# Kernel optimization log

Hardware: AMD Instinct MI355X
Metric: run time of the kernel (lower is better)

## Reference

```python
import jax, jax.numpy as jnp
import numpy as np

T, IN, INTER, OUT = 4096, 1024, 1024, 1024

def setup_inputs() -> dict:
    key = jax.random.key(0)
    ks = jax.random.split(key, 11)
    s_in = 1.0 / np.sqrt(IN)
    s_int = 1.0 / np.sqrt(INTER)
    return {
        "x": jax.random.normal(ks[0], (T, IN), dtype=jnp.float32),
        "d_gamma": jax.random.uniform(ks[1], (T, T), dtype=jnp.float32),
        "Wq": jax.random.uniform(ks[2], (IN, INTER), jnp.float32, -s_in, s_in),
        "bq": jax.random.uniform(ks[3], (INTER,), jnp.float32, -s_in, s_in),
        "Wk": jax.random.uniform(ks[4], (IN, INTER), jnp.float32, -s_in, s_in),
        "bk": jax.random.uniform(ks[5], (INTER,), jnp.float32, -s_in, s_in),
        "Wv": jax.random.uniform(ks[6], (IN, INTER), jnp.float32, -s_in, s_in),
        "bv": jax.random.uniform(ks[7], (INTER,), jnp.float32, -s_in, s_in),
        "Wr": jax.random.uniform(ks[8], (INTER, OUT), jnp.float32, -s_int, s_int),
        "br": jax.random.uniform(ks[9], (OUT,), jnp.float32, -s_int, s_int),
        "prelu_a": jnp.asarray(0.25, dtype=jnp.float32),
    }

def reference(x, d_gamma, Wq, bq, Wk, bk, Wv, bv, Wr, br, prelu_a):
    num_node = x.shape[0]
    xr = x.reshape(T, IN)
    q = xr @ Wq + bq                      # [T, INTER]
    k = xr @ Wk + bk                      # [T, INTER]
    v = xr @ Wv + bv                      # [T, INTER]
    scores = q @ k.T                      # [T, T] retention scores
    retained = (d_gamma * scores) @ v     # decay-masked aggregation, [T, INTER]
    out = retained @ Wr + br              # [T, OUT]
    out = jnp.where(out >= 0, out, prelu_a * out)  # PReLU
    return out.reshape(num_node, -1)
```

## Files before the change

### kernel.cpp

```cpp
#include <hip/hip_runtime.h>

#define TT 4096
#define DIN 1024

typedef _Float16 f16;
typedef __attribute__((ext_vector_type(8))) _Float16 f16x8;
typedef __attribute__((ext_vector_type(4))) _Float16 f16x4;
typedef __attribute__((ext_vector_type(4))) float f32x4;

__device__ f16 g_xh[TT * DIN];
__device__ f16 g_wqkvT[3 * DIN * DIN];
__device__ f16 g_wrT[DIN * DIN];
__device__ f16 g_q[TT * DIN];
__device__ f16 g_k[TT * DIN];
__device__ f16 g_v[TT * DIN];
__device__ f16 g_vT[DIN * TT];
__device__ f16 g_sg[(size_t)TT * TT];
__device__ f16 g_part[4][TT * DIN];
__device__ f16 g_ret[TT * DIN];

__global__ __launch_bounds__(256) void prep_cast_x(const float* __restrict__ x) {
    int i = (blockIdx.x * 256 + threadIdx.x) * 8;
    f32x4 a = *(const f32x4*)&x[i];
    f32x4 b = *(const f32x4*)&x[i + 4];
    f16x8 o;
#pragma unroll
    for (int j = 0; j < 4; ++j) { o[j] = (f16)a[j]; o[j + 4] = (f16)b[j]; }
    *(f16x8*)&g_xh[i] = o;
}

__global__ void prep_transpose(const float* __restrict__ Wq, const float* __restrict__ Wk,
                               const float* __restrict__ Wv, const float* __restrict__ Wr) {
    int idx = blockIdx.x * 256 + threadIdx.x;
    int which = blockIdx.y;
    const float* src = (which == 0) ? Wq : (which == 1) ? Wk : (which == 2) ? Wv : Wr;
    f16* dst = (which < 3) ? (g_wqkvT + (size_t)which * DIN * DIN) : g_wrT;
    int j = idx >> 10, k = idx & 1023;
    dst[idx] = (f16)src[k * DIN + j];
}

__global__ __launch_bounds__(256) void transpose_v() {
    __shared__ f16 t[64][72];
    const int bc = blockIdx.x;
    const int br = blockIdx.y;
    const int tdx = threadIdx.x;
    const int r0 = tdx >> 3;
    const int c8 = (tdx & 7) * 8;
#pragma unroll
    for (int p = 0; p < 2; ++p) {
        int r = r0 + p * 32;
        *(f16x8*)&t[r][c8] = *(const f16x8*)&g_v[(size_t)(br * 64 + r) * DIN + bc * 64 + c8];
    }
    __syncthreads();
#pragma unroll
    for (int p = 0; p < 2; ++p) {
        int c = r0 + p * 32;
        f16x8 v;
#pragma unroll
        for (int j = 0; j < 8; ++j) v[j] = t[c8 + j][c];
        *(f16x8*)&g_vT[(size_t)(bc * 64 + c) * TT + br * 64 + c8] = v;
    }
}

__global__ __launch_bounds__(256) void gamma_mult(const float* __restrict__ gamma) {
    const size_t total = (size_t)TT * TT;
    const size_t stride = (size_t)gridDim.x * 256 * 8;
    for (size_t i = ((size_t)blockIdx.x * 256 + threadIdx.x) * 8; i < total; i += stride) {
        f16x8 sv = *(const f16x8*)&g_sg[i];
        f32x4 g0 = *(const f32x4*)&gamma[i];
        f32x4 g1 = *(const f32x4*)&gamma[i + 4];
        f16x8 o;
#pragma unroll
        for (int j = 0; j < 4; ++j) {
            o[j]     = (f16)((float)sv[j] * g0[j]);
            o[j + 4] = (f16)((float)sv[j + 4] * g1[j]);
        }
        *(f16x8*)&g_sg[i] = o;
    }
}

__device__ __forceinline__ void gload_lds16(const void* g, void* l) {
    __builtin_amdgcn_global_load_lds(
        (const __attribute__((address_space(1))) unsigned int*)g,
        (__attribute__((address_space(3))) unsigned int*)l,
        16, 0, 0);
}

template <int EPI>
__global__ __launch_bounds__(512, 2) void gemm8(const float* __restrict__ bq,
                                                const float* __restrict__ bk,
                                                const float* __restrict__ bv) {
    constexpr int NT  = (EPI == 3) ? 4 : 16;
    constexpr int ld2A = (EPI == 2) ? 8192 : 2048;
    constexpr int ld2B = (EPI == 2) ? 8192 : 2048;

    const f16* Ap = (EPI == 0) ? g_xh : (EPI == 1) ? g_q : (EPI == 2) ? g_sg : g_ret;
    const f16* Bp = (EPI == 0) ? g_wqkvT : (EPI == 1) ? g_k : (EPI == 2) ? g_vT : g_wrT;
    const int kb_base = (EPI == 2) ? blockIdx.z * 2048
                      : (EPI == 3) ? blockIdx.z * 512 : 0;

    __shared__ __align__(16) char smem[131072];

    const int t = threadIdx.x;
    const int w = t >> 6, l = t & 63;
    const int wr = w >> 2, wc = w & 3;
    const int fr = l & 15;
    const int fkb = (l >> 4) * 16;

    const int nx = gridDim.x;
    const int lin = blockIdx.y * nx + blockIdx.x;
    const int cpx = (nx * gridDim.y) >> 3;
    const int sw = (lin & 7) * cpx + (lin >> 3);
    const int bx = sw % nx, by = sw / nx;
    const int arow0 = by * 256;
    const int bcol0 = bx * 256;

    auto stage = [&](const f16* M, int ld2, int row0, int kb0, int dstoff) {
#pragma unroll
        for (int r = 0; r < 2; ++r) {
            int off = r * 8192 + w * 1024;
            int row = (off + l * 16) >> 7;
            int cb  = (l & 7) * 16;
            int scb = cb ^ ((row & 7) << 4);
            const char* src = (const char*)M + (size_t)(row0 + row) * ld2 + kb0 + scb;
            gload_lds16(src, smem + dstoff + off);
        }
    };

    auto ldsA = [&](int c, int m, int ks) -> f16x8 {
        int lr = m * 16 + fr;
        int kb = ks * 64 + fkb;
        return *(const f16x8*)(smem + c * 65536 + wr * 16384 + lr * 128 + (kb ^ ((lr & 7) << 4)));
    };
    auto ldsB = [&](int c, int n, int ks) -> f16x8 {
        int lc = (wc & 1) * 64 + n * 16 + fr;
        int kb = ks * 64 + fkb;
        return *(const f16x8*)(smem + c * 65536 + 32768 + (wc >> 1) * 16384 + lc * 128 + (kb ^ ((lc & 7) << 4)));
    };

#define KB(kt) (kb_base + (kt) * 128)

    stage(Ap, ld2A, arow0,       KB(0), 0);
    stage(Ap, ld2A, arow0 + 128, KB(0), 16384);
    stage(Bp, ld2B, bcol0,       KB(0), 32768);
    stage(Bp, ld2B, bcol0 + 128, KB(0), 49152);
    stage(Bp, ld2B, bcol0,       KB(1), 65536 + 32768);
    stage(Bp, ld2B, bcol0 + 128, KB(1), 65536 + 49152);

    f32x4 acc[8][4] = {};
    f16x8 bf[4][2];

#define GPHASE(MB, STAGE_STMT)                                              \
    {                                                                       \
        f16x8 af[2][2];                                                     \
        _Pragma("unroll") for (int i = 0; i < 2; ++i)                       \
            _Pragma("unroll") for (int ks = 0; ks < 2; ++ks)                \
                af[i][ks] = ldsA(c, (MB) + i, ks);                          \
        STAGE_STMT;                                                         \
        __builtin_amdgcn_s_barrier();                                       \
        __builtin_amdgcn_s_setprio(1);                                      \
        _Pragma("unroll") for (int i = 0; i < 2; ++i)                       \
            _Pragma("unroll") for (int n = 0; n < 4; ++n)                   \
                _Pragma("unroll") for (int ks = 0; ks < 2; ++ks)            \
                    acc[(MB) + i][n] = __builtin_amdgcn_mfma_f32_16x16x32_f16( \
                        af[i][ks], bf[n][ks], acc[(MB) + i][n], 0, 0, 0);   \
        __builtin_amdgcn_s_setprio(0);                                      \
        __builtin_amdgcn_s_barrier();                                       \
    }

    for (int kt = 0; kt < NT; ++kt) {
        const int c = kt & 1;
        if (kt == NT - 1) asm volatile("s_waitcnt vmcnt(0)" ::: "memory");
        else              asm volatile("s_waitcnt vmcnt(4)" ::: "memory");
        __builtin_amdgcn_s_barrier();
#pragma unroll
        for (int n = 0; n < 4; ++n)
#pragma unroll
            for (int ks = 0; ks < 2; ++ks) bf[n][ks] = ldsB(c, n, ks);
        GPHASE(0, if (kt + 1 < NT) stage(Ap, ld2A, arow0,       KB(kt + 1), (c ^ 1) * 65536))
        GPHASE(2, if (kt + 1 < NT) stage(Ap, ld2A, arow0 + 128, KB(kt + 1), (c ^ 1) * 65536 + 16384))
        GPHASE(4, if (kt + 2 < NT) stage(Bp, ld2B, bcol0,       KB(kt + 2), c * 65536 + 32768))
        GPHASE(6, if (kt + 2 < NT) stage(Bp, ld2B, bcol0 + 128, KB(kt + 2), c * 65536 + 49152))
    }
#undef GPHASE
#undef KB

    __syncthreads();
    char* slice = smem + w * 16384;
    const int rb = (l >> 4) * 4;
    const int crow0 = arow0 + wr * 128;
    const int ccol0 = bcol0 + wc * 64;

    const int sel = (EPI == 0) ? (bx >> 2) : 0;
    const float* bias0 = (EPI == 0) ? ((sel == 0) ? bq : (sel == 1) ? bk : bv) : nullptr;
    const int cb0 = (EPI == 0) ? (ccol0 - sel * 1024) : ccol0;

#pragma unroll
    for (int m = 0; m < 8; ++m)
#pragma unroll
        for (int n = 0; n < 4; ++n) {
            float bsum = 0.f;
            if constexpr (EPI == 0) bsum = bias0[cb0 + n * 16 + fr];
#pragma unroll
            for (int j = 0; j < 4; ++j) {
                const int lr = m * 16 + rb + j;
                const int lcb = (n * 16 + fr) * 2;
                *(f16*)(slice + lr * 128 + (lcb ^ ((lr & 7) << 4))) = (f16)(acc[m][n][j] + bsum);
            }
        }
    asm volatile("s_waitcnt lgkmcnt(0)" ::: "memory");
    __builtin_amdgcn_sched_barrier(0);

    f16* dst;
    int ld;
    if constexpr (EPI == 0)      { dst = (sel == 0) ? g_q : (sel == 1) ? g_k : g_v; ld = 1024; }
    else if constexpr (EPI == 1) { dst = g_sg;               ld = TT;   }
    else                         { dst = g_part[blockIdx.z]; ld = 1024; }

#pragma unroll
    for (int i = 0; i < 16; ++i) {
        const int r  = i * 8 + (l >> 3);
        const int cb = (l & 7) * 16;
        f16x8 vv = *(const f16x8*)(slice + r * 128 + (cb ^ ((r & 7) << 4)));
        *(f16x8*)&dst[(size_t)(crow0 + r) * ld + cb0 + (l & 7) * 8] = vv;
    }
}

__global__ __launch_bounds__(256) void reduce_parts() {
    size_t i = (size_t)(blockIdx.x * 256 + threadIdx.x) * 8;
    f16x8 a = *(const f16x8*)&g_part[0][i];
    f16x8 b = *(const f16x8*)&g_part[1][i];
    f16x8 cc = *(const f16x8*)&g_part[2][i];
    f16x8 d = *(const f16x8*)&g_part[3][i];
    f16x8 o;
#pragma unroll
    for (int j = 0; j < 8; ++j)
        o[j] = (f16)((float)a[j] + (float)b[j] + (float)cc[j] + (float)d[j]);
    *(f16x8*)&g_ret[i] = o;
}

__global__ __launch_bounds__(256) void reduce_out(const float* __restrict__ br,
                                                  const float* __restrict__ prelu_a,
                                                  float* __restrict__ out) {
    size_t i = (size_t)(blockIdx.x * 256 + threadIdx.x) * 8;
    f16x8 a = *(const f16x8*)&g_part[0][i];
    f16x8 b = *(const f16x8*)&g_part[1][i];
    f16x8 cc = *(const f16x8*)&g_part[2][i];
    f16x8 d = *(const f16x8*)&g_part[3][i];
    const float pa = *prelu_a;
    const int col = (int)(i & 1023);
    const f32x4 b0 = *(const f32x4*)&br[col];
    const f32x4 b1 = *(const f32x4*)&br[col + 4];
    f32x4 o0, o1;
#pragma unroll
    for (int j = 0; j < 4; ++j) {
        float s = (float)a[j] + (float)b[j] + (float)cc[j] + (float)d[j] + b0[j];
        o0[j] = (s >= 0.f) ? s : pa * s;
    }
#pragma unroll
    for (int j = 0; j < 4; ++j) {
        float s = (float)a[j + 4] + (float)b[j + 4] + (float)cc[j + 4] + (float)d[j + 4] + b1[j];
        o1[j] = (s >= 0.f) ? s : pa * s;
    }
    *(f32x4*)&out[i] = o0;
    *(f32x4*)&out[i + 4] = o1;
}

extern "C" void kernel_launch(void* const* d_in, const int* in_sizes, int n_in,
                              void* d_out, int out_size, void* d_ws, size_t ws_size,
                              hipStream_t stream) {
    const float* x     = (const float*)d_in[0];
    const float* gamma = (const float*)d_in[1];
    const float* Wq    = (const float*)d_in[2];
    const float* bq    = (const float*)d_in[3];
    const float* Wk    = (const float*)d_in[4];
    const float* bk    = (const float*)d_in[5];
    const float* Wv    = (const float*)d_in[6];
    const float* bv    = (const float*)d_in[7];
    const float* Wr    = (const float*)d_in[8];
    const float* br    = (const float*)d_in[9];
    const float* pa    = (const float*)d_in[10];
    float* out = (float*)d_out;

    prep_cast_x<<<TT * DIN / 8 / 256, 256, 0, stream>>>(x);
    prep_transpose<<<dim3(DIN * DIN / 256, 4), 256, 0, stream>>>(Wq, Wk, Wv, Wr);

    gemm8<0><<<dim3(12, 16), 512, 0, stream>>>(bq, bk, bv);
    transpose_v<<<dim3(16, 64), 256, 0, stream>>>();
    gemm8<1><<<dim3(16, 16), 512, 0, stream>>>(bq, bk, bv);
    gamma_mult<<<2048, 256, 0, stream>>>(gamma);
    gemm8<2><<<dim3(4, 16, 4), 512, 0, stream>>>(bq, bk, bv);
    reduce_parts<<<TT * DIN / 8 / 256, 256, 0, stream>>>();
    gemm8<3><<<dim3(4, 16, 4), 512, 0, stream>>>(bq, bk, bv);
    reduce_out<<<TT * DIN / 8 / 256, 256, 0, stream>>>(br, pa, out);
}
```

Before: 200.5 us.

## Triple-buffer A tiles in GEMM and tile the weight transpose through LDS

The GEMM's shared-memory plan changes so that A tiles use three buffers and B tiles keep two. Both operands are now prefetched two k-steps ahead, and the wait threshold is relaxed so more global loads stay in flight behind the MFMA work. Separately, the weight transpose now stages 64x64 tiles through shared memory, so reads and writes are coalesced and vectorised instead of strided. The cost is 160KB of LDS per GEMM block, which uses the whole CU's LDS.

Result: faster. 189.7 us (-5.4%).

```diff
diff --git a/kernel.cpp b/kernel.cpp
--- a/kernel.cpp
+++ b/kernel.cpp
@@ -29,14 +29,31 @@
     *(f16x8*)&g_xh[i] = o;
 }
 
-__global__ void prep_transpose(const float* __restrict__ Wq, const float* __restrict__ Wk,
-                               const float* __restrict__ Wv, const float* __restrict__ Wr) {
-    int idx = blockIdx.x * 256 + threadIdx.x;
-    int which = blockIdx.y;
+__global__ __launch_bounds__(256) void prep_transpose(const float* __restrict__ Wq,
+                                                      const float* __restrict__ Wk,
+                                                      const float* __restrict__ Wv,
+                                                      const float* __restrict__ Wr) {
+    __shared__ float tt[64][68];
+    const int which = blockIdx.z;
     const float* src = (which == 0) ? Wq : (which == 1) ? Wk : (which == 2) ? Wv : Wr;
     f16* dst = (which < 3) ? (g_wqkvT + (size_t)which * DIN * DIN) : g_wrT;
-    int j = idx >> 10, k = idx & 1023;
-    dst[idx] = (f16)src[k * DIN + j];
+    const int t = threadIdx.x;
+    const int r = t >> 2;
+    const int c0 = (t & 3) * 4;
+#pragma unroll
+    for (int ch = 0; ch < 4; ++ch)
+        *(f32x4*)&tt[r][c0 + ch * 16] =
+            *(const f32x4*)&src[(size_t)(blockIdx.y * 64 + r) * DIN + blockIdx.x * 64 + c0 + ch * 16];
+    __syncthreads();
+#pragma unroll
+    for (int p = 0; p < 2; ++p) {
+        const int j  = (t >> 3) + p * 32;
+        const int k0 = (t & 7) * 8;
+        f16x8 o;
+#pragma unroll
+        for (int jj = 0; jj < 8; ++jj) o[jj] = (f16)tt[k0 + jj][j];
+        *(f16x8*)&dst[(size_t)(blockIdx.x * 64 + j) * DIN + blockIdx.y * 64 + k0] = o;
+    }
 }
 
 __global__ __launch_bounds__(256) void transpose_v() {
@@ -99,7 +116,7 @@
     const int kb_base = (EPI == 2) ? blockIdx.z * 2048
                       : (EPI == 3) ? blockIdx.z * 512 : 0;
 
-    __shared__ __align__(16) char smem[131072];
+    __shared__ __align__(16) char smem[163840];
 
     const int t = threadIdx.x;
     const int w = t >> 6, l = t & 63;
@@ -127,25 +144,27 @@
         }
     };
 
-    auto ldsA = [&](int c, int m, int ks) -> f16x8 {
+    auto ldsA = [&](int c3, int m, int ks) -> f16x8 {
         int lr = m * 16 + fr;
         int kb = ks * 64 + fkb;
-        return *(const f16x8*)(smem + c * 65536 + wr * 16384 + lr * 128 + (kb ^ ((lr & 7) << 4)));
+        return *(const f16x8*)(smem + c3 * 32768 + wr * 16384 + lr * 128 + (kb ^ ((lr & 7) << 4)));
     };
-    auto ldsB = [&](int c, int n, int ks) -> f16x8 {
+    auto ldsB = [&](int c2, int n, int ks) -> f16x8 {
         int lc = (wc & 1) * 64 + n * 16 + fr;
         int kb = ks * 64 + fkb;
-        return *(const f16x8*)(smem + c * 65536 + 32768 + (wc >> 1) * 16384 + lc * 128 + (kb ^ ((lc & 7) << 4)));
+        return *(const f16x8*)(smem + 98304 + c2 * 32768 + (wc >> 1) * 16384 + lc * 128 + (kb ^ ((lc & 7) << 4)));
     };
 
 #define KB(kt) (kb_base + (kt) * 128)
 
     stage(Ap, ld2A, arow0,       KB(0), 0);
     stage(Ap, ld2A, arow0 + 128, KB(0), 16384);
-    stage(Bp, ld2B, bcol0,       KB(0), 32768);
-    stage(Bp, ld2B, bcol0 + 128, KB(0), 49152);
-    stage(Bp, ld2B, bcol0,       KB(1), 65536 + 32768);
-    stage(Bp, ld2B, bcol0 + 128, KB(1), 65536 + 49152);
+    stage(Bp, ld2B, bcol0,       KB(0), 98304);
+    stage(Bp, ld2B, bcol0 + 128, KB(0), 98304 + 16384);
+    stage(Ap, ld2A, arow0,       KB(1), 32768);
+    stage(Ap, ld2A, arow0 + 128, KB(1), 32768 + 16384);
+    stage(Bp, ld2B, bcol0,       KB(1), 98304 + 32768);
+    stage(Bp, ld2B, bcol0 + 128, KB(1), 98304 + 32768 + 16384);
 
     f32x4 acc[8][4] = {};
     f16x8 bf[4][2];
@@ -155,7 +174,7 @@
         f16x8 af[2][2];                                                     \
         _Pragma("unroll") for (int i = 0; i < 2; ++i)                       \
             _Pragma("unroll") for (int ks = 0; ks < 2; ++ks)                \
-                af[i][ks] = ldsA(c, (MB) + i, ks);                          \
+                af[i][ks] = ldsA(c3, (MB) + i, ks);                         \
         STAGE_STMT;                                                         \
         __builtin_amdgcn_s_barrier();                                       \
         __builtin_amdgcn_s_setprio(1);                                      \
@@ -169,18 +188,20 @@
     }
 
     for (int kt = 0; kt < NT; ++kt) {
-        const int c = kt & 1;
+        const int c3 = kt % 3;
+        const int a3 = (kt + 2) % 3;
+        const int c2 = kt & 1;
         if (kt == NT - 1) asm volatile("s_waitcnt vmcnt(0)" ::: "memory");
-        else              asm volatile("s_waitcnt vmcnt(4)" ::: "memory");
+        else              asm volatile("s_waitcnt vmcnt(8)" ::: "memory");
         __builtin_amdgcn_s_barrier();
 #pragma unroll
         for (int n = 0; n < 4; ++n)
 #pragma unroll
-            for (int ks = 0; ks < 2; ++ks) bf[n][ks] = ldsB(c, n, ks);
-        GPHASE(0, if (kt + 1 < NT) stage(Ap, ld2A, arow0,       KB(kt + 1), (c ^ 1) * 65536))
-        GPHASE(2, if (kt + 1 < NT) stage(Ap, ld2A, arow0 + 128, KB(kt + 1), (c ^ 1) * 65536 + 16384))
-        GPHASE(4, if (kt + 2 < NT) stage(Bp, ld2B, bcol0,       KB(kt + 2), c * 65536 + 32768))
-        GPHASE(6, if (kt + 2 < NT) stage(Bp, ld2B, bcol0 + 128, KB(kt + 2), c * 65536 + 49152))
+            for (int ks = 0; ks < 2; ++ks) bf[n][ks] = ldsB(c2, n, ks);
+        GPHASE(0, if (kt + 2 < NT) stage(Ap, ld2A, arow0,       KB(kt + 2), a3 * 32768))
+        GPHASE(2, if (kt + 2 < NT) stage(Ap, ld2A, arow0 + 128, KB(kt + 2), a3 * 32768 + 16384))
+        GPHASE(4, if (kt + 2 < NT) stage(Bp, ld2B, bcol0,       KB(kt + 2), 98304 + c2 * 32768))
+        GPHASE(6, if (kt + 2 < NT) stage(Bp, ld2B, bcol0 + 128, KB(kt + 2), 98304 + c2 * 32768 + 16384))
     }
 #undef GPHASE
 #undef KB
@@ -216,7 +237,6 @@
     if constexpr (EPI == 0)      { dst = (sel == 0) ? g_q : (sel == 1) ? g_k : g_v; ld = 1024; }
     else if constexpr (EPI == 1) { dst = g_sg;               ld = TT;   }
     else                         { dst = g_part[blockIdx.z]; ld = 1024; }
-
 #pragma unroll
     for (int i = 0; i < 16; ++i) {
         const int r  = i * 8 + (l >> 3);
@@ -283,7 +303,7 @@
     float* out = (float*)d_out;
 
     prep_cast_x<<<TT * DIN / 8 / 256, 256, 0, stream>>>(x);
-    prep_transpose<<<dim3(DIN * DIN / 256, 4), 256, 0, stream>>>(Wq, Wk, Wv, Wr);
+    prep_transpose<<<dim3(16, 16, 4), 256, 0, stream>>>(Wq, Wk, Wv, Wr);
 
     gemm8<0><<<dim3(12, 16), 512, 0, stream>>>(bq, bk, bv);
     transpose_v<<<dim3(16, 64), 256, 0, stream>>>();
```

## Fuse V transpose into QKV GEMM epilogue and tile weight transpose via LDS

Applied to the files above, without the earlier changes.

The QKV projection epilogue now writes V directly in transposed layout through a swizzled LDS slice, which removes the separate transpose_v kernel and the g_v intermediate buffer. The weight-transpose prep kernel is rewritten to stage 64x64 tiles in shared memory, so its reads and writes are coalesced instead of strided one-element gathers. This saves one launch and one full round trip of V through global memory. In exchange, the LDS layout in the V epilogue is different and its bank-conflict behaviour may change.

New measurement: 182.9 us. 8.8% less time.

```diff
diff --git a/kernel.cpp b/kernel.cpp
--- a/kernel.cpp
+++ b/kernel.cpp
@@ -13,7 +13,6 @@
 __device__ f16 g_wrT[DIN * DIN];
 __device__ f16 g_q[TT * DIN];
 __device__ f16 g_k[TT * DIN];
-__device__ f16 g_v[TT * DIN];
 __device__ f16 g_vT[DIN * TT];
 __device__ f16 g_sg[(size_t)TT * TT];
 __device__ f16 g_part[4][TT * DIN];
@@ -29,36 +28,30 @@
     *(f16x8*)&g_xh[i] = o;
 }
 
-__global__ void prep_transpose(const float* __restrict__ Wq, const float* __restrict__ Wk,
-                               const float* __restrict__ Wv, const float* __restrict__ Wr) {
-    int idx = blockIdx.x * 256 + threadIdx.x;
-    int which = blockIdx.y;
+__global__ __launch_bounds__(256) void prep_transpose(const float* __restrict__ Wq,
+                                                      const float* __restrict__ Wk,
+                                                      const float* __restrict__ Wv,
+                                                      const float* __restrict__ Wr) {
+    __shared__ float tt[64][68];
+    const int which = blockIdx.z;
     const float* src = (which == 0) ? Wq : (which == 1) ? Wk : (which == 2) ? Wv : Wr;
     f16* dst = (which < 3) ? (g_wqkvT + (size_t)which * DIN * DIN) : g_wrT;
-    int j = idx >> 10, k = idx & 1023;
-    dst[idx] = (f16)src[k * DIN + j];
-}
-
-__global__ __launch_bounds__(256) void transpose_v() {
-    __shared__ f16 t[64][72];
-    const int bc = blockIdx.x;
-    const int br = blockIdx.y;
-    const int tdx = threadIdx.x;
-    const int r0 = tdx >> 3;
-    const int c8 = (tdx & 7) * 8;
+    const int t = threadIdx.x;
+    const int r = t >> 2;
+    const int c0 = (t & 3) * 4;
+#pragma unroll
+    for (int ch = 0; ch < 4; ++ch)
+        *(f32x4*)&tt[r][c0 + ch * 16] =
+            *(const f32x4*)&src[(size_t)(blockIdx.y * 64 + r) * DIN + blockIdx.x * 64 + c0 + ch * 16];
+    __syncthreads();
 #pragma unroll
     for (int p = 0; p < 2; ++p) {
-        int r = r0 + p * 32;
-        *(f16x8*)&t[r][c8] = *(const f16x8*)&g_v[(size_t)(br * 64 + r) * DIN + bc * 64 + c8];
-    }
-    __syncthreads();
-#pragma unroll
-    for (int p = 0; p < 2; ++p) {
-        int c = r0 + p * 32;
-        f16x8 v;
-#pragma unroll
-        for (int j = 0; j < 8; ++j) v[j] = t[c8 + j][c];
-        *(f16x8*)&g_vT[(size_t)(bc * 64 + c) * TT + br * 64 + c8] = v;
+        const int j  = (t >> 3) + p * 32;
+        const int k0 = (t & 7) * 8;
+        f16x8 o;
+#pragma unroll
+        for (int jj = 0; jj < 8; ++jj) o[jj] = (f16)tt[k0 + jj][j];
+        *(f16x8*)&dst[(size_t)(blockIdx.x * 64 + j) * DIN + blockIdx.y * 64 + k0] = o;
     }
 }
 
@@ -195,34 +188,56 @@
     const float* bias0 = (EPI == 0) ? ((sel == 0) ? bq : (sel == 1) ? bk : bv) : nullptr;
     const int cb0 = (EPI == 0) ? (ccol0 - sel * 1024) : ccol0;
 
-#pragma unroll
-    for (int m = 0; m < 8; ++m)
-#pragma unroll
-        for (int n = 0; n < 4; ++n) {
-            float bsum = 0.f;
-            if constexpr (EPI == 0) bsum = bias0[cb0 + n * 16 + fr];
-#pragma unroll
-            for (int j = 0; j < 4; ++j) {
-                const int lr = m * 16 + rb + j;
-                const int lcb = (n * 16 + fr) * 2;
-                *(f16*)(slice + lr * 128 + (lcb ^ ((lr & 7) << 4))) = (f16)(acc[m][n][j] + bsum);
+    if (EPI == 0 && sel == 2) {
+#pragma unroll
+        for (int m = 0; m < 8; ++m)
+#pragma unroll
+            for (int n = 0; n < 4; ++n) {
+                const int cl = n * 16 + fr;
+                const float bsum = bias0[cb0 + cl];
+#pragma unroll
+                for (int j = 0; j < 4; ++j) {
+                    const int rw = m * 16 + rb + j;
+                    *(f16*)(slice + cl * 256 + ((rw * 2) ^ ((cl & 7) << 4))) = (f16)(acc[m][n][j] + bsum);
+                }
             }
+        asm volatile("s_waitcnt lgkmcnt(0)" ::: "memory");
+        __builtin_amdgcn_sched_barrier(0);
+#pragma unroll
+        for (int i = 0; i < 16; ++i) {
+            const int cv = i * 4 + (l >> 4);
+            const int b0 = (l & 15) * 16;
+            f16x8 vv = *(const f16x8*)(slice + cv * 256 + (b0 ^ ((cv & 7) << 4)));
+            *(f16x8*)&g_vT[(size_t)(cb0 + cv) * TT + crow0 + (l & 15) * 8] = vv;
         }
-    asm volatile("s_waitcnt lgkmcnt(0)" ::: "memory");
-    __builtin_amdgcn_sched_barrier(0);
-
-    f16* dst;
-    int ld;
-    if constexpr (EPI == 0)      { dst = (sel == 0) ? g_q : (sel == 1) ? g_k : g_v; ld = 1024; }
-    else if constexpr (EPI == 1) { dst = g_sg;               ld = TT;   }
-    else                         { dst = g_part[blockIdx.z]; ld = 1024; }
-
-#pragma unroll
-    for (int i = 0; i < 16; ++i) {
-        const int r  = i * 8 + (l >> 3);
-        const int cb = (l & 7) * 16;
-        f16x8 vv = *(const f16x8*)(slice + r * 128 + (cb ^ ((r & 7) << 4)));
-        *(f16x8*)&dst[(size_t)(crow0 + r) * ld + cb0 + (l & 7) * 8] = vv;
+    } else {
+#pragma unroll
+        for (int m = 0; m < 8; ++m)
+#pragma unroll
+            for (int n = 0; n < 4; ++n) {
+                float bsum = 0.f;
+                if constexpr (EPI == 0) bsum = bias0[cb0 + n * 16 + fr];
+#pragma unroll
+                for (int j = 0; j < 4; ++j) {
+                    const int lr = m * 16 + rb + j;
+                    const int lcb = (n * 16 + fr) * 2;
+                    *(f16*)(slice + lr * 128 + (lcb ^ ((lr & 7) << 4))) = (f16)(acc[m][n][j] + bsum);
+                }
+            }
+        asm volatile("s_waitcnt lgkmcnt(0)" ::: "memory");
+        __builtin_amdgcn_sched_barrier(0);
+        f16* dst;
+        int ld;
+        if constexpr (EPI == 0)      { dst = (sel == 0) ? g_q : g_k; ld = 1024; }
+        else if constexpr (EPI == 1) { dst = g_sg;               ld = TT;   }
+        else                         { dst = g_part[blockIdx.z]; ld = 1024; }
+#pragma unroll
+        for (int i = 0; i < 16; ++i) {
+            const int r  = i * 8 + (l >> 3);
+            const int cb = (l & 7) * 16;
+            f16x8 vv = *(const f16x8*)(slice + r * 128 + (cb ^ ((r & 7) << 4)));
+            *(f16x8*)&dst[(size_t)(crow0 + r) * ld + cb0 + (l & 7) * 8] = vv;
+        }
     }
 }
 
@@ -283,10 +298,9 @@
     float* out = (float*)d_out;
 
     prep_cast_x<<<TT * DIN / 8 / 256, 256, 0, stream>>>(x);
-    prep_transpose<<<dim3(DIN * DIN / 256, 4), 256, 0, stream>>>(Wq, Wk, Wv, Wr);
+    prep_transpose<<<dim3(16, 16, 4), 256, 0, stream>>>(Wq, Wk, Wv, Wr);
 
     gemm8<0><<<dim3(12, 16), 512, 0, stream>>>(bq, bk, bv);
-    transpose_v<<<dim3(16, 64), 256, 0, stream>>>();
     gemm8<1><<<dim3(16, 16), 512, 0, stream>>>(bq, bk, bv);
     gamma_mult<<<2048, 256, 0, stream>>>(gamma);
     gemm8<2><<<dim3(4, 16, 4), 512, 0, stream>>>(bq, bk, bv);
```
